# Performance work log

Hardware: AMD Instinct MI355X
Metric: run time of the kernel (lower is better)

## Reference

```python
import jax, jax.numpy as jnp
import numpy as np

SEQ_LEN = 28
EMBED = 28
HIDDEN = 256
OUT = 10
BATCH = 32768


def _orthogonal(key, rows, cols):
    # mimic torch orthogonal init via QR
    a = jax.random.normal(key, (max(rows, cols), min(rows, cols)), dtype=jnp.float32)
    q, r = jnp.linalg.qr(a)
    q = q * jnp.sign(jnp.diagonal(r))
    if rows < cols:
        q = q.T
    return q[:rows, :cols]


def setup_inputs() -> dict:
    key = jax.random.key(0)
    ks = jax.random.split(key, 7)
    seq = jax.random.normal(ks[0], (BATCH, SEQ_LEN, EMBED), dtype=jnp.float32)
    bound1 = 1.0 / np.sqrt(EMBED)
    bound2 = 1.0 / np.sqrt(HIDDEN)
    return {
        "seq": seq,
        "W1": _orthogonal(ks[1], HIDDEN, EMBED),            # linear1.weight [H, E]
        "b1": jax.random.uniform(ks[2], (HIDDEN,), minval=-bound1, maxval=bound1),
        "W2": _orthogonal(ks[3], HIDDEN, HIDDEN),           # linear2.weight [H, H]
        "b2": jax.random.uniform(ks[4], (HIDDEN,), minval=-bound2, maxval=bound2),
        "W3": _orthogonal(ks[5], OUT, HIDDEN),              # linear3.weight [O, H]
        "b3": jax.random.uniform(ks[6], (OUT,), minval=-bound2, maxval=bound2),
    }


def reference(seq, W1, b1, W2, b2, W3, b3):
    B = seq.shape[0]
    seq = seq.reshape(B, SEQ_LEN, -1)
    # precompute input projection for all steps: [B, T, H]
    x_proj = jnp.einsum("bte,he->bth", seq, W1) + b1
    h0 = jnp.zeros((B, HIDDEN), dtype=seq.dtype)

    def step(h, xp_t):
        h = jnp.tanh(xp_t + h @ W2.T + b2)
        return h, None

    h, _ = jax.lax.scan(step, h0, jnp.swapaxes(x_proj, 0, 1))  # scan over T
    return h @ W3.T + b3
```

## Files before the change

### kernel.cpp

```cpp
#include <hip/hip_runtime.h>
#include <hip/hip_bf16.h>

#define T_LEN 28
#define EMB   28
#define HID   256
#define NOUT  10
#define BATCH 32768

typedef _Float16 f16x8 __attribute__((ext_vector_type(8)));
typedef _Float16 f16x4 __attribute__((ext_vector_type(4)));
typedef float    f32x4 __attribute__((ext_vector_type(4)));

__global__ __launch_bounds__(256) void prep_kernel(
    const float* __restrict__ W1, const float* __restrict__ W2,
    const float* __restrict__ b1, const float* __restrict__ b2,
    _Float16* __restrict__ W2A, _Float16* __restrict__ W1A) {
    int idx = blockIdx.x * 256 + threadIdx.x;
    if (idx < 65536) {
        int i  = idx & 7;
        int l  = (idx >> 3) & 63;
        int kb = (idx >> 9) & 7;
        int jt = idx >> 12;
        int j  = jt * 16 + (l & 15);
        int k  = kb * 32 + (l >> 4) * 8 + i;
        W2A[idx] = (_Float16)W2[j * HID + k];
    }
    if (idx < 8192) {
        int i  = idx & 7;
        int l  = (idx >> 3) & 63;
        int jt = idx >> 9;
        int j  = jt * 16 + (l & 15);
        int k  = (l >> 4) * 8 + i;
        float v = (k < EMB) ? W1[j * EMB + k] : (k == EMB ? (b1[j] + b2[j]) : 0.f);
        W1A[idx] = (_Float16)v;
    }
}

__global__ __launch_bounds__(256, 2) void rnn_kernel(
    const float* __restrict__ seq,
    const _Float16* __restrict__ W2A,
    const _Float16* __restrict__ W1A,
    const float* __restrict__ W3,
    const float* __restrict__ b3,
    float* __restrict__ out)
{
    __shared__ __align__(16) char lds[T_LEN * 1024 + 2 * 8192];
    char* const xls = lds;
    char* const hls = lds + T_LEN * 1024;

    const int tid = threadIdx.x;
    const int l   = tid & 63;
    const int wv  = tid >> 6;
    const int lr  = l & 15;
    const int lg  = l >> 4;
    const int r0  = blockIdx.x * 16;

    for (int idx = tid; idx < 16 * T_LEN * 4; idx += 256) {
        int i  = idx / 112;
        int tc = idx - i * 112;
        int t  = tc >> 2;
        int c  = tc & 3;
        const float* sp = seq + (size_t)(r0 + i) * (T_LEN * EMB) + t * EMB + c * 8;
        f32x4 f0 = *(const f32x4*)sp;
        f32x4 f1;
        if (c < 3) f1 = *(const f32x4*)(sp + 4);
        else       f1 = (f32x4){1.f, 0.f, 0.f, 0.f};
        f16x8 v;
#pragma unroll
        for (int q = 0; q < 4; ++q) { v[q] = (_Float16)f0[q]; v[4 + q] = (_Float16)f1[q]; }
        *(f16x8*)(xls + ((t * 4 + c) * 16 + i) * 16) = v;
    }

    f16x8 w2f[4][8];
#pragma unroll
    for (int a = 0; a < 4; ++a)
#pragma unroll
        for (int kb = 0; kb < 8; ++kb)
            w2f[a][kb] = *(const f16x8*)(W2A + ((((wv * 4 + a) * 8 + kb) * 64 + l) * 8));
    f16x8 w1f[4];
#pragma unroll
    for (int a = 0; a < 4; ++a)
        w1f[a] = *(const f16x8*)(W1A + (((wv * 4 + a) * 64 + l) * 8));

    __syncthreads();

    for (int t = 0; t < T_LEN; ++t) {
        f32x4 acc[4];
#pragma unroll
        for (int a = 0; a < 4; ++a) acc[a] = (f32x4){0.f, 0.f, 0.f, 0.f};

        f16x8 xB = *(const f16x8*)(xls + t * 1024 + l * 16);
#pragma unroll
        for (int a = 0; a < 4; ++a)
            acc[a] = __builtin_amdgcn_mfma_f32_16x16x32_f16(w1f[a], xB, acc[a], 0, 0, 0);

        if (t > 0) {
            const char* rp = hls + ((t + 1) & 1) * 8192 + l * 16;
            f16x8 hB = *(const f16x8*)rp;
#pragma unroll
            for (int kb = 0; kb < 8; ++kb) {
                f16x8 hN;
                if (kb < 7) hN = *(const f16x8*)(rp + (kb + 1) * 1024);
#pragma unroll
                for (int a = 0; a < 4; ++a)
                    acc[a] = __builtin_amdgcn_mfma_f32_16x16x32_f16(w2f[a][kb], hB, acc[a], 0, 0, 0);
                hB = hN;
            }
        }

        char* wb = hls + (t & 1) * 8192;
#pragma unroll
        for (int a = 0; a < 4; ++a) {
            f16x4 hv;
#pragma unroll
            for (int r = 0; r < 4; ++r) {
                float y = acc[a][r];
                float e = __builtin_amdgcn_exp2f(2.8853900817779268f * y);
                float rc = __builtin_amdgcn_rcpf(e + 1.f);
                hv[r] = (_Float16)__builtin_fmaf(-2.f, rc, 1.f);
            }
            int c = (wv * 4 + a) * 2 + (lg >> 1);
            *(f16x4*)(wb + (c * 16 + lr) * 16 + (lg & 1) * 8) = hv;
        }
        __syncthreads();
    }

    const char* hb = hls + ((T_LEN - 1) & 1) * 8192;
    for (int idx = tid; idx < 16 * NOUT; idx += 256) {
        int i = idx / NOUT;
        int o = idx - i * NOUT;
        float s = b3[o];
#pragma unroll
        for (int c = 0; c < 32; ++c) {
            f16x8 hv  = *(const f16x8*)(hb + (c * 16 + i) * 16);
            f32x4 w0  = *(const f32x4*)(W3 + o * HID + c * 8);
            f32x4 w1v = *(const f32x4*)(W3 + o * HID + c * 8 + 4);
#pragma unroll
            for (int q = 0; q < 4; ++q)
                s += (float)hv[q] * w0[q] + (float)hv[4 + q] * w1v[q];
        }
        out[(size_t)(r0 + i) * NOUT + o] = s;
    }
}

extern "C" void kernel_launch(void* const* d_in, const int* in_sizes, int n_in,
                              void* d_out, int out_size, void* d_ws, size_t ws_size,
                              hipStream_t stream) {
    const float* seq = (const float*)d_in[0];
    const float* W1  = (const float*)d_in[1];
    const float* b1  = (const float*)d_in[2];
    const float* W2  = (const float*)d_in[3];
    const float* b2  = (const float*)d_in[4];
    const float* W3  = (const float*)d_in[5];
    const float* b3  = (const float*)d_in[6];
    float* outp = (float*)d_out;

    _Float16* W2A = (_Float16*)d_ws;
    _Float16* W1A = (_Float16*)((char*)d_ws + 65536 * sizeof(_Float16));

    prep_kernel<<<256, 256, 0, stream>>>(W1, W2, b1, b2, W2A, W1A);
    rnn_kernel<<<BATCH / 16, 256, 0, stream>>>(seq, W2A, W1A, W3, b3, outp);
}
```

Measured before the change: 151.0 us.

## Interleave two batch tiles per block to overlap tanh with MFMA

Each block now handles 32 rows as two 16-row tiles, alternating phases so that the tanh and h-store of one tile are interleaved with the W2 MFMAs of the other. The sequence input is no longer staged in LDS; it is loaded directly from global memory each step into registers. This cuts LDS use and hides the serial tanh latency behind matrix work. In exchange it raises register pressure and adds per-step global load latency.

```diff
diff --git a/kernel.cpp b/kernel.cpp
--- a/kernel.cpp
+++ b/kernel.cpp
@@ -44,32 +44,14 @@
     const float* __restrict__ b3,
     float* __restrict__ out)
 {
-    __shared__ __align__(16) char lds[T_LEN * 1024 + 2 * 8192];
-    char* const xls = lds;
-    char* const hls = lds + T_LEN * 1024;
+    __shared__ __align__(16) char hls[2][8192];
 
     const int tid = threadIdx.x;
     const int l   = tid & 63;
     const int wv  = tid >> 6;
     const int lr  = l & 15;
     const int lg  = l >> 4;
-    const int r0  = blockIdx.x * 16;
-
-    for (int idx = tid; idx < 16 * T_LEN * 4; idx += 256) {
-        int i  = idx / 112;
-        int tc = idx - i * 112;
-        int t  = tc >> 2;
-        int c  = tc & 3;
-        const float* sp = seq + (size_t)(r0 + i) * (T_LEN * EMB) + t * EMB + c * 8;
-        f32x4 f0 = *(const f32x4*)sp;
-        f32x4 f1;
-        if (c < 3) f1 = *(const f32x4*)(sp + 4);
-        else       f1 = (f32x4){1.f, 0.f, 0.f, 0.f};
-        f16x8 v;
-#pragma unroll
-        for (int q = 0; q < 4; ++q) { v[q] = (_Float16)f0[q]; v[4 + q] = (_Float16)f1[q]; }
-        *(f16x8*)(xls + ((t * 4 + c) * 16 + i) * 16) = v;
-    }
+    const int r0  = blockIdx.x * 32;
 
     f16x8 w2f[4][8];
 #pragma unroll
@@ -82,57 +64,100 @@
     for (int a = 0; a < 4; ++a)
         w1f[a] = *(const f16x8*)(W1A + (((wv * 4 + a) * 64 + l) * 8));
 
+    int wOff[4];
+#pragma unroll
+    for (int a = 0; a < 4; ++a)
+        wOff[a] = ((((wv * 4 + a) * 2 + (lg >> 1)) * 16) + lr) * 16 + (lg & 1) * 8;
+
+    const float* rowA = seq + (size_t)(r0 + lr) * (T_LEN * EMB);
+    const float* rowB = seq + (size_t)(r0 + 16 + lr) * (T_LEN * EMB);
+
+    auto load_x = [&](const float* rowp, int t) -> f16x8 {
+        const float* sp = rowp + t * EMB + lg * 8;
+        f32x4 f0 = *(const f32x4*)sp;
+        f32x4 f1 = (f32x4){1.f, 0.f, 0.f, 0.f};
+        if (lg < 3) f1 = *(const f32x4*)(sp + 4);
+        f16x8 v;
+#pragma unroll
+        for (int q = 0; q < 4; ++q) { v[q] = (_Float16)f0[q]; v[4 + q] = (_Float16)f1[q]; }
+        return v;
+    };
+
+    auto tanh4 = [&](const f32x4& a4) -> f16x4 {
+        f16x4 hv;
+#pragma unroll
+        for (int r = 0; r < 4; ++r) {
+            float e  = __builtin_amdgcn_exp2f(2.8853900817779268f * a4[r]);
+            float rc = __builtin_amdgcn_rcpf(e + 1.f);
+            hv[r] = (_Float16)__builtin_fmaf(-2.f, rc, 1.f);
+        }
+        return hv;
+    };
+
+    const f32x4 z = (f32x4){0.f, 0.f, 0.f, 0.f};
+    f32x4 accA[4], accB[4];
+
+    auto do_phase = [&](f32x4 (&acc)[4], f32x4 (&accPrev)[4],
+                        const char* rbase, char* wbase, const f16x8& xf) {
+        f16x8 hf[8];
+#pragma unroll
+        for (int kb = 0; kb < 8; ++kb)
+            hf[kb] = *(const f16x8*)(rbase + kb * 1024);
+#pragma unroll
+        for (int kb = 0; kb < 8; ++kb) {
+#pragma unroll
+            for (int a = 0; a < 4; ++a)
+                acc[a] = __builtin_amdgcn_mfma_f32_16x16x32_f16(
+                             w2f[a][kb], hf[kb], (kb == 0) ? z : acc[a], 0, 0, 0);
+            if (kb & 1) {
+                int a2 = kb >> 1;
+                *(f16x4*)(wbase + wOff[a2]) = tanh4(accPrev[a2]);
+            }
+        }
+#pragma unroll
+        for (int a = 0; a < 4; ++a)
+            acc[a] = __builtin_amdgcn_mfma_f32_16x16x32_f16(w1f[a], xf, acc[a], 0, 0, 0);
+    };
+
+    {
+        f16x8 xA = load_x(rowA, 0);
+        f16x8 xB = load_x(rowB, 0);
+#pragma unroll
+        for (int a = 0; a < 4; ++a) {
+            accA[a] = __builtin_amdgcn_mfma_f32_16x16x32_f16(w1f[a], xA, z, 0, 0, 0);
+            accB[a] = __builtin_amdgcn_mfma_f32_16x16x32_f16(w1f[a], xB, z, 0, 0, 0);
+        }
+#pragma unroll
+        for (int a = 0; a < 4; ++a)
+            *(f16x4*)(hls[0] + wOff[a]) = tanh4(accA[a]);
+    }
     __syncthreads();
 
-    for (int t = 0; t < T_LEN; ++t) {
-        f32x4 acc[4];
-#pragma unroll
-        for (int a = 0; a < 4; ++a) acc[a] = (f32x4){0.f, 0.f, 0.f, 0.f};
+    for (int t = 1; t < T_LEN; ++t) {
+        f16x8 xA = load_x(rowA, t);
+        f16x8 xB = load_x(rowB, t);
 
-        f16x8 xB = *(const f16x8*)(xls + t * 1024 + l * 16);
-#pragma unroll
-        for (int a = 0; a < 4; ++a)
-            acc[a] = __builtin_amdgcn_mfma_f32_16x16x32_f16(w1f[a], xB, acc[a], 0, 0, 0);
+        do_phase(accA, accB, hls[0] + l * 16, hls[1], xA);
+        __syncthreads();
 
-        if (t > 0) {
-            const char* rp = hls + ((t + 1) & 1) * 8192 + l * 16;
-            f16x8 hB = *(const f16x8*)rp;
-#pragma unroll
-            for (int kb = 0; kb < 8; ++kb) {
-                f16x8 hN;
-                if (kb < 7) hN = *(const f16x8*)(rp + (kb + 1) * 1024);
-#pragma unroll
-                for (int a = 0; a < 4; ++a)
-                    acc[a] = __builtin_amdgcn_mfma_f32_16x16x32_f16(w2f[a][kb], hB, acc[a], 0, 0, 0);
-                hB = hN;
-            }
-        }
-
-        char* wb = hls + (t & 1) * 8192;
-#pragma unroll
-        for (int a = 0; a < 4; ++a) {
-            f16x4 hv;
-#pragma unroll
-            for (int r = 0; r < 4; ++r) {
-                float y = acc[a][r];
-                float e = __builtin_amdgcn_exp2f(2.8853900817779268f * y);
-                float rc = __builtin_amdgcn_rcpf(e + 1.f);
-                hv[r] = (_Float16)__builtin_fmaf(-2.f, rc, 1.f);
-            }
-            int c = (wv * 4 + a) * 2 + (lg >> 1);
-            *(f16x4*)(wb + (c * 16 + lr) * 16 + (lg & 1) * 8) = hv;
-        }
+        do_phase(accB, accA, hls[1] + l * 16, hls[0], xB);
         __syncthreads();
     }
 
-    const char* hb = hls + ((T_LEN - 1) & 1) * 8192;
-    for (int idx = tid; idx < 16 * NOUT; idx += 256) {
+#pragma unroll
+    for (int a = 0; a < 4; ++a)
+        *(f16x4*)(hls[1] + wOff[a]) = tanh4(accB[a]);
+    __syncthreads();
+
+    for (int idx = tid; idx < 32 * NOUT; idx += 256) {
         int i = idx / NOUT;
         int o = idx - i * NOUT;
+        const char* hb = hls[i >> 4];
+        int ii = i & 15;
         float s = b3[o];
 #pragma unroll
         for (int c = 0; c < 32; ++c) {
-            f16x8 hv  = *(const f16x8*)(hb + (c * 16 + i) * 16);
+            f16x8 hv  = *(const f16x8*)(hb + c * 256 + ii * 16);
             f32x4 w0  = *(const f32x4*)(W3 + o * HID + c * 8);
             f32x4 w1v = *(const f32x4*)(W3 + o * HID + c * 8 + 4);
 #pragma unroll
@@ -159,5 +184,5 @@
     _Float16* W1A = (_Float16*)((char*)d_ws + 65536 * sizeof(_Float16));
 
     prep_kernel<<<256, 256, 0, stream>>>(W1, W2, b1, b2, W2A, W1A);
-    rnn_kernel<<<BATCH / 16, 256, 0, stream>>>(seq, W2A, W1A, W3, b3, outp);
+    rnn_kernel<<<BATCH / 32, 256, 0, stream>>>(seq, W2A, W1A, W3, b3, outp);
 }
```

Result: slower. 171.5 us (+13.6%).
